# Performance work log

Hardware: AMD Instinct MI355X
Metric: run time of the kernel (lower is better)

## Reference

```python
import jax, jax.numpy as jnp
import numpy as np

B, S, E = 2, 2048, 1024
D_ATTN, H = 1024, 16
HD = D_ATTN // H
SCALE = 1.0 / np.sqrt(D_ATTN)
ROPE_BASE = 10000.0


def setup_inputs() -> dict:
    key = jax.random.key(0)
    ks = jax.random.split(key, 7)
    def w(k, shape, scale):
        return jax.random.normal(k, shape, dtype=jnp.float32) * scale
    return {
        "q": w(ks[0], (B, S, E), 1.0),
        "k": w(ks[1], (B, S, E), 1.0),
        "v": w(ks[2], (B, S, E), 1.0),
        "Wq": w(ks[3], (D_ATTN, E), E ** -0.5),
        "Wk": w(ks[4], (D_ATTN, E), E ** -0.5),
        "Wv": w(ks[5], (D_ATTN, E), E ** -0.5),
        "Wo": w(ks[6], (E, D_ATTN), D_ATTN ** -0.5),
    }


def _rope(x):
    # x: [B, H, S, HD]; interleaved-pair rotary embedding over the seq axis
    s, d = x.shape[2], x.shape[3]
    half = d // 2
    inv_freq = 1.0 / (ROPE_BASE ** (jnp.arange(half, dtype=jnp.float32) * 2.0 / d))
    ang = jnp.arange(s, dtype=jnp.float32)[:, None] * inv_freq[None, :]  # [S, half]
    cos, sin = jnp.cos(ang), jnp.sin(ang)
    xr = x.reshape(x.shape[:-1] + (half, 2))
    x0, x1 = xr[..., 0], xr[..., 1]
    o0 = x0 * cos - x1 * sin
    o1 = x0 * sin + x1 * cos
    return jnp.stack([o0, o1], axis=-1).reshape(x.shape)


def reference(q, k, v, Wq, Wk, Wv, Wo):
    # linear projections (nn.Linear with weight [out, in]): y = x @ W^T
    qh = (q @ Wq.T).reshape(B, S, H, HD).transpose(0, 2, 1, 3)  # [B,H,S,HD]
    kh = (k @ Wk.T).reshape(B, S, H, HD).transpose(0, 2, 1, 3)
    vh = (v @ Wv.T).reshape(B, S, H, HD).transpose(0, 2, 1, 3)
    qh = _rope(qh)
    kh = _rope(kh)
    # shifted-causal mask: disallow j >= i (diagonal masked), except (0,0) allowed
    i = jnp.arange(S)[:, None]
    j = jnp.arange(S)[None, :]
    masked = j >= i                              # triu incl. diagonal
    masked = masked.at[0, 0].set(False)          # keep (0,0) so row 0 isn't all -inf
    scores = jnp.einsum("bhsd,bhtd->bhst", qh, kh) * SCALE
    scores = jnp.where(masked, -jnp.inf, scores)
    probs = jax.nn.softmax(scores, axis=-1)      # dropout omitted (eval mode)
    ctx = jnp.einsum("bhst,bhtd->bhsd", probs, vh)
    ctx = ctx.transpose(0, 2, 1, 3).reshape(B, S, D_ATTN)
    return ctx @ Wo.T
```

## Files before the change

### kernel.cpp

```cpp
#include <hip/hip_runtime.h>
#include <hip/hip_bf16.h>

#define BATCH 2
#define SEQ   2048
#define EMB   1024
#define DATTN 1024
#define NH    16
#define HD    64
#define MM    (BATCH*SEQ)
#define SCALE 0.03125f
#define MINIT -1.0e30f
#define ROPE_COEF 0.41524101186f

using bf16x8 = __attribute__((ext_vector_type(8))) short;
using f32x4  = __attribute__((ext_vector_type(4))) float;

__device__ inline short f2bf(float x) {
    __hip_bfloat16 b = __float2bfloat16(x);
    return *reinterpret_cast<short*>(&b);
}

__device__ inline void gl_lds16(const short* g, short* l) {
    __builtin_amdgcn_global_load_lds(
        (const __attribute__((address_space(1))) unsigned int*)g,
        (__attribute__((address_space(3))) unsigned int*)l, 16, 0, 0);
}

__global__ __launch_bounds__(256)
void cvt_all(const float* __restrict__ q, const float* __restrict__ k,
             const float* __restrict__ v,
             const float* __restrict__ Wq, const float* __restrict__ Wk,
             const float* __restrict__ Wv, const float* __restrict__ Wo,
             short* __restrict__ dst)
{
    const long QKV = (long)MM * EMB;
    const long WSZ = (long)DATTN * EMB;
    const long i = ((long)blockIdx.x * 256 + threadIdx.x) * 4;
    const float* s;
    long off;
    if (i < 3 * QKV) {
        const int seg = (int)(i / QKV);
        off = i - (long)seg * QKV;
        s = (seg == 0) ? q : (seg == 1) ? k : v;
    } else {
        const long j = i - 3 * QKV;
        const int seg = (int)(j / WSZ);
        off = j - (long)seg * WSZ;
        s = (seg == 0) ? Wq : (seg == 1) ? Wk : (seg == 2) ? Wv : Wo;
    }
    float4 x = *(const float4*)(s + off);
    short4 y;
    y.x = f2bf(x.x); y.y = f2bf(x.y); y.z = f2bf(x.z); y.w = f2bf(x.w);
    *(short4*)(dst + i) = y;
}

__device__ inline void stage_tile(const short* g, short* lds, int wave, int lane) {
    #pragma unroll
    for (int qq = 0; qq < 2; ++qq) {
        const int r = wave * 32 + qq * 16 + (lane >> 2);
        gl_lds16(g + (long)r * EMB + (lane & 3) * 8, lds + (wave * 2 + qq) * 512);
    }
}

__global__ __launch_bounds__(256)
void gemm_proj_bf16(const short* __restrict__ qb, const short* __restrict__ kb,
                    const short* __restrict__ vb,
                    const short* __restrict__ wqb, const short* __restrict__ wkb,
                    const short* __restrict__ wvb,
                    short* __restrict__ Qb, short* __restrict__ Kb,
                    short* __restrict__ Vtb)
{
    const short* A; const short* B;
    if (blockIdx.z == 0)      { A = qb; B = wqb; }
    else if (blockIdx.z == 1) { A = kb; B = wkb; }
    else                      { A = vb; B = wvb; }

    __shared__ short sA[128 * 32];
    __shared__ short sB[128 * 32];

    const int tid  = threadIdx.x;
    const int wave = tid >> 6, lane = tid & 63;
    const int quad = lane >> 4, l16 = lane & 15;
    const int wm = (wave >> 1) * 64, wn = (wave & 1) * 64;
    const long m0 = (long)blockIdx.x * 128, n0 = (long)blockIdx.y * 128;

    f32x4 acc[4][4];
    #pragma unroll
    for (int i = 0; i < 4; ++i)
        #pragma unroll
        for (int j = 0; j < 4; ++j) acc[i][j] = (f32x4){0.f, 0.f, 0.f, 0.f};

    for (int kt = 0; kt < EMB; kt += 32) {
        __syncthreads();
        stage_tile(A + m0 * EMB + kt, sA, wave, lane);
        stage_tile(B + n0 * EMB + kt, sB, wave, lane);
        __syncthreads();

        bf16x8 af[4], bfr[4];
        #pragma unroll
        for (int rt = 0; rt < 4; ++rt)
            af[rt] = *(const bf16x8*)&sA[(wm + rt * 16 + l16) * 32 + quad * 8];
        #pragma unroll
        for (int ct = 0; ct < 4; ++ct)
            bfr[ct] = *(const bf16x8*)&sB[(wn + ct * 16 + l16) * 32 + quad * 8];
        #pragma unroll
        for (int rt = 0; rt < 4; ++rt)
            #pragma unroll
            for (int ct = 0; ct < 4; ++ct)
                acc[rt][ct] = __builtin_amdgcn_mfma_f32_16x16x32_bf16(
                    af[rt], bfr[ct], acc[rt][ct], 0, 0, 0);
    }

    if (blockIdx.z < 2) {
        short* C = (blockIdx.z == 0) ? Qb : Kb;
        const float scl = (blockIdx.z == 0) ? SCALE : 1.0f;
        const int odd = l16 & 1;
        #pragma unroll
        for (int ct = 0; ct < 4; ++ct) {
            const long col = n0 + wn + ct * 16 + l16;
            const int hh = (int)(col >> 6), dd = (int)(col & (HD - 1));
            const float invf = exp2f(-ROPE_COEF * (float)(dd >> 1));
            #pragma unroll
            for (int rt = 0; rt < 4; ++rt) {
                #pragma unroll
                for (int reg = 0; reg < 4; ++reg) {
                    const long row = m0 + wm + rt * 16 + quad * 4 + reg;
                    const int bb = (int)(row >> 11), ss = (int)(row & (SEQ - 1));
                    const float val = acc[rt][ct][reg];
                    const float prt = __shfl_xor(val, 1, 64);
                    float sn, cs;
                    __sincosf((float)ss * invf, &sn, &cs);
                    const float o = odd ? (prt * sn + val * cs)
                                        : (val * cs - prt * sn);
                    C[(((long)(bb * NH + hh)) << 17) + ((long)ss << 6) + dd] =
                        f2bf(o * scl);
                }
            }
        }
    } else {
        #pragma unroll
        for (int rt = 0; rt < 4; ++rt) {
            #pragma unroll
            for (int ct = 0; ct < 4; ++ct) {
                const long row0 = m0 + wm + rt * 16 + quad * 4;
                const long col  = n0 + wn + ct * 16 + l16;
                const int bb = (int)(row0 >> 11), ss = (int)(row0 & (SEQ - 1));
                const int hh = (int)(col >> 6),   dd = (int)(col & (HD - 1));
                short4 s4;
                s4.x = f2bf(acc[rt][ct][0]); s4.y = f2bf(acc[rt][ct][1]);
                s4.z = f2bf(acc[rt][ct][2]); s4.w = f2bf(acc[rt][ct][3]);
                *(short4*)&Vtb[(((long)(bb * NH + hh)) << 17) + ((long)dd << 11) + ss] = s4;
            }
        }
    }
}

__global__ __launch_bounds__(256)
void gemm_out_bf16(const short* __restrict__ Ab, const short* __restrict__ Bb,
                   float* __restrict__ C)
{
    __shared__ short sA[128 * 32];
    __shared__ short sB[128 * 32];

    const int tid  = threadIdx.x;
    const int wave = tid >> 6, lane = tid & 63;
    const int quad = lane >> 4, l16 = lane & 15;
    const int wm = (wave >> 1) * 64, wn = (wave & 1) * 64;
    const long m0 = (long)blockIdx.x * 128, n0 = (long)blockIdx.y * 128;

    f32x4 acc[4][4];
    #pragma unroll
    for (int i = 0; i < 4; ++i)
        #pragma unroll
        for (int j = 0; j < 4; ++j) acc[i][j] = (f32x4){0.f, 0.f, 0.f, 0.f};

    for (int kt = 0; kt < DATTN; kt += 32) {
        __syncthreads();
        stage_tile(Ab + m0 * DATTN + kt, sA, wave, lane);
        stage_tile(Bb + n0 * DATTN + kt, sB, wave, lane);
        __syncthreads();

        bf16x8 af[4], bfr[4];
        #pragma unroll
        for (int rt = 0; rt < 4; ++rt)
            af[rt] = *(const bf16x8*)&sA[(wm + rt * 16 + l16) * 32 + quad * 8];
        #pragma unroll
        for (int ct = 0; ct < 4; ++ct)
            bfr[ct] = *(const bf16x8*)&sB[(wn + ct * 16 + l16) * 32 + quad * 8];
        #pragma unroll
        for (int rt = 0; rt < 4; ++rt)
            #pragma unroll
            for (int ct = 0; ct < 4; ++ct)
                acc[rt][ct] = __builtin_amdgcn_mfma_f32_16x16x32_bf16(
                    af[rt], bfr[ct], acc[rt][ct], 0, 0, 0);
    }

    #pragma unroll
    for (int rt = 0; rt < 4; ++rt) {
        #pragma unroll
        for (int ct = 0; ct < 4; ++ct) {
            #pragma unroll
            for (int reg = 0; reg < 4; ++reg) {
                const long row = m0 + wm + rt * 16 + quad * 4 + reg;
                const long col = n0 + wn + ct * 16 + l16;
                C[row * EMB + col] = acc[rt][ct][reg];
            }
        }
    }
}

#define LDP 72

__global__ __launch_bounds__(256, 1)
void flash_attn_mfma(const short* __restrict__ Qb,
                     const short* __restrict__ Kb,
                     const short* __restrict__ Vtb,
                     short* __restrict__ ctx)
{
    const int id = blockIdx.x;
    const int r  = id & 7;
    const int q8 = id >> 3;
    const int ts = q8 & 31;
    const int pi = q8 >> 5;
    const int p  = r + 8 * pi;
    const int b  = p >> 4, h = p & 15;
    const int t  = 31 - ts;
    const int tid = threadIdx.x;
    const int wave = tid >> 6, lane = tid & 63;
    const int quad = lane >> 4, l16 = lane & 15;
    const int r0 = t * 64;

    __shared__ short sk2[2][64 * LDP];
    __shared__ short sv2[2][64 * LDP];
    __shared__ short sp[4][16 * LDP];

    const long base = ((long)(b * NH + h)) << 17;

    const int iq = r0 + wave * 16 + l16;
    bf16x8 qf[2];
    #pragma unroll
    for (int tt = 0; tt < 2; ++tt)
        qf[tt] = *(const bf16x8*)(Qb + base + (long)iq * HD + tt * 32 + quad * 8);

    f32x4 acc_o[4];
    #pragma unroll
    for (int ct = 0; ct < 4; ++ct) acc_o[ct] = (f32x4){0.f, 0.f, 0.f, 0.f};
    float mq = MINIT, lq = 0.f;

    const int njt = (t + 2) >> 1;

    #pragma unroll 1
    for (int jt = 0; jt < njt; ++jt) {
        const int jbase = jt * 128;

        __syncthreads();
        #pragma unroll
        for (int c = 0; c < 4; ++c) {
            int cc   = c * 256 + tid;
            int half = cc >> 9;
            int row  = (cc >> 3) & 63;
            int off  = (cc & 7) * 8;
            int4 tK = *(const int4*)(Kb + base
                + (long)(jbase + half * 64 + row) * HD + off);
            *(int4*)&sk2[half][row * LDP + off] = tK;
            int4 tV = *(const int4*)(Vtb + base
                + ((long)row << 11) + jbase + half * 64 + off);
            *(int4*)&sv2[half][row * LDP + off] = tV;
        }
        __syncthreads();

        #pragma unroll
        for (int half = 0; half < 2; ++half) {
            const int jt2 = 2 * jt + half;
            if (jt2 > t) continue;
            const int jb2 = jbase + half * 64;
            const short* skh = sk2[half];
            const short* svh = sv2[half];

            bf16x8 kf[4][2], vf[4][2];
            #pragma unroll
            for (int ct = 0; ct < 4; ++ct) {
                kf[ct][0] = *(const bf16x8*)&skh[(ct * 16 + l16) * LDP + quad * 8];
                kf[ct][1] = *(const bf16x8*)&skh[(ct * 16 + l16) * LDP + 32 + quad * 8];
                vf[ct][0] = *(const bf16x8*)&svh[(ct * 16 + l16) * LDP + quad * 8];
                vf[ct][1] = *(const bf16x8*)&svh[(ct * 16 + l16) * LDP + 32 + quad * 8];
            }

            f32x4 s[4];
            #pragma unroll
            for (int ct = 0; ct < 4; ++ct) {
                f32x4 z = (f32x4){0.f, 0.f, 0.f, 0.f};
                z = __builtin_amdgcn_mfma_f32_16x16x32_bf16(kf[ct][0], qf[0], z, 0, 0, 0);
                z = __builtin_amdgcn_mfma_f32_16x16x32_bf16(kf[ct][1], qf[1], z, 0, 0, 0);
                s[ct] = z;
            }

            if (jt2 == t) {
                #pragma unroll
                for (int ct = 0; ct < 4; ++ct)
                    #pragma unroll
                    for (int rr = 0; rr < 4; ++rr) {
                        const int j = jb2 + ct * 16 + quad * 4 + rr;
                        const bool ok = (j < iq) || (iq == 0 && j == 0);
                        if (!ok) s[ct][rr] = -INFINITY;
                    }
            }

            float mx = MINIT;
            #pragma unroll
            for (int ct = 0; ct < 4; ++ct)
                #pragma unroll
                for (int rr = 0; rr < 4; ++rr) mx = fmaxf(mx, s[ct][rr]);
            mx = fmaxf(mx, __shfl_xor(mx, 16, 64));
            mx = fmaxf(mx, __shfl_xor(mx, 32, 64));
            const float mn = fmaxf(mq, mx);
            const float alpha = __expf(mq - mn);
            mq = mn;
            float ss = 0.f;
            #pragma unroll
            for (int ct = 0; ct < 4; ++ct)
                #pragma unroll
                for (int rr = 0; rr < 4; ++rr) {
                    const float e = __expf(s[ct][rr] - mn);
                    s[ct][rr] = e;
                    ss += e;
                }
            ss += __shfl_xor(ss, 16, 64);
            ss += __shfl_xor(ss, 32, 64);
            lq = lq * alpha + ss;

            short* pw = sp[wave];
            #pragma unroll
            for (int ct = 0; ct < 4; ++ct) {
                short4 p4;
                p4.x = f2bf(s[ct][0]); p4.y = f2bf(s[ct][1]);
                p4.z = f2bf(s[ct][2]); p4.w = f2bf(s[ct][3]);
                *(short4*)&pw[l16 * LDP + ct * 16 + quad * 4] = p4;
            }

            #pragma unroll
            for (int ct = 0; ct < 4; ++ct)
                #pragma unroll
                for (int rr = 0; rr < 4; ++rr) acc_o[ct][rr] *= alpha;

            bf16x8 pf0 = *(const bf16x8*)&pw[l16 * LDP + quad * 8];
            bf16x8 pf1 = *(const bf16x8*)&pw[l16 * LDP + 32 + quad * 8];
            #pragma unroll
            for (int ct = 0; ct < 4; ++ct) {
                acc_o[ct] = __builtin_amdgcn_mfma_f32_16x16x32_bf16(
                    vf[ct][0], pf0, acc_o[ct], 0, 0, 0);
                acc_o[ct] = __builtin_amdgcn_mfma_f32_16x16x32_bf16(
                    vf[ct][1], pf1, acc_o[ct], 0, 0, 0);
            }
        }
    }

    const float inv = 1.f / lq;
    short* orow = ctx + (long)(b * SEQ + iq) * DATTN + h * HD;
    #pragma unroll
    for (int ct = 0; ct < 4; ++ct) {
        short4 o4;
        o4.x = f2bf(acc_o[ct][0] * inv);
        o4.y = f2bf(acc_o[ct][1] * inv);
        o4.z = f2bf(acc_o[ct][2] * inv);
        o4.w = f2bf(acc_o[ct][3] * inv);
        *(short4*)&orow[ct * 16 + quad * 4] = o4;
    }
}

extern "C" void kernel_launch(void* const* d_in, const int* in_sizes, int n_in,
                              void* d_out, int out_size, void* d_ws, size_t ws_size,
                              hipStream_t stream) {
    const float* q  = (const float*)d_in[0];
    const float* k  = (const float*)d_in[1];
    const float* v  = (const float*)d_in[2];
    const float* Wq = (const float*)d_in[3];
    const float* Wk = (const float*)d_in[4];
    const float* Wv = (const float*)d_in[5];
    const float* Wo = (const float*)d_in[6];
    float* out = (float*)d_out;

    const long QKV = (long)MM * EMB;
    const long WSZ = (long)DATTN * EMB;
    short* basep = (short*)d_ws;
    short* qb  = basep;
    short* kb  = qb + QKV;
    short* vb  = kb + QKV;
    short* wqb = vb + QKV;
    short* wkb = wqb + WSZ;
    short* wvb = wkb + WSZ;
    short* wob = wvb + WSZ;
    short* Qb  = wob + WSZ;
    short* Kb  = Qb + QKV;
    short* Vtb = Kb + QKV;
    short* ctx = Vtb + QKV;

    cvt_all<<<16384, 256, 0, stream>>>(q, k, v, Wq, Wk, Wv, Wo, qb);

    gemm_proj_bf16<<<dim3(MM / 128, DATTN / 128, 3), 256, 0, stream>>>(
        qb, kb, vb, wqb, wkb, wvb, Qb, Kb, Vtb);

    flash_attn_mfma<<<1024, 256, 0, stream>>>(Qb, Kb, Vtb, ctx);

    gemm_out_bf16<<<dim3(MM / 128, EMB / 128), 256, 0, stream>>>(ctx, wob, out);
}
```

Baseline: 237.3 us.

## Pair causal query tiles per block and prefetch K/V tiles into registers

Each attention block now handles two query tiles, a short one (ta) and its mirror long one (31-ta). Both share each staged K/V tile, which balances causal work across blocks and halves K/V loads per query. The next K/V stage is loaded into registers while the current tile is computed, overlapping global loads with MFMA work. The launch bound is raised to 2 blocks per CU. The grid halves to 512 blocks, and the doubled accumulators and Q fragments raise register pressure.

After: 274.4 us. 1.16x slower.

```diff
diff --git a/kernel.cpp b/kernel.cpp
--- a/kernel.cpp
+++ b/kernel.cpp
@@ -211,7 +211,7 @@
 
 #define LDP 72
 
-__global__ __launch_bounds__(256, 1)
+__global__ __launch_bounds__(256, 2)
 void flash_attn_mfma(const short* __restrict__ Qb,
                      const short* __restrict__ Kb,
                      const short* __restrict__ Vtb,
@@ -219,61 +219,152 @@
 {
     const int id = blockIdx.x;
     const int r  = id & 7;
-    const int q8 = id >> 3;
-    const int ts = q8 & 31;
-    const int pi = q8 >> 5;
+    const int q6 = id >> 3;
+    const int ta = q6 & 15;
+    const int pi = q6 >> 4;
     const int p  = r + 8 * pi;
     const int b  = p >> 4, h = p & 15;
-    const int t  = 31 - ts;
+    const int tA = ta;
+    const int tB = 31 - ta;
     const int tid = threadIdx.x;
     const int wave = tid >> 6, lane = tid & 63;
     const int quad = lane >> 4, l16 = lane & 15;
-    const int r0 = t * 64;
 
     __shared__ short sk2[2][64 * LDP];
     __shared__ short sv2[2][64 * LDP];
-    __shared__ short sp[4][16 * LDP];
+    __shared__ short spA[4][16 * LDP];
+    __shared__ short spB[4][16 * LDP];
 
     const long base = ((long)(b * NH + h)) << 17;
 
-    const int iq = r0 + wave * 16 + l16;
-    bf16x8 qf[2];
-    #pragma unroll
-    for (int tt = 0; tt < 2; ++tt)
-        qf[tt] = *(const bf16x8*)(Qb + base + (long)iq * HD + tt * 32 + quad * 8);
-
-    f32x4 acc_o[4];
-    #pragma unroll
-    for (int ct = 0; ct < 4; ++ct) acc_o[ct] = (f32x4){0.f, 0.f, 0.f, 0.f};
-    float mq = MINIT, lq = 0.f;
-
-    const int njt = (t + 2) >> 1;
+    const int iqA = tA * 64 + wave * 16 + l16;
+    const int iqB = tB * 64 + wave * 16 + l16;
+    bf16x8 qfA[2], qfB[2];
+    #pragma unroll
+    for (int tt = 0; tt < 2; ++tt) {
+        qfA[tt] = *(const bf16x8*)(Qb + base + (long)iqA * HD + tt * 32 + quad * 8);
+        qfB[tt] = *(const bf16x8*)(Qb + base + (long)iqB * HD + tt * 32 + quad * 8);
+    }
+
+    f32x4 accA[4], accB[4];
+    #pragma unroll
+    for (int ct = 0; ct < 4; ++ct) {
+        accA[ct] = (f32x4){0.f, 0.f, 0.f, 0.f};
+        accB[ct] = (f32x4){0.f, 0.f, 0.f, 0.f};
+    }
+    float mqA = MINIT, lqA = 0.f, mqB = MINIT, lqB = 0.f;
+
+    const int nr = (tB + 2) >> 1;
+
+    auto attn_tile = [&](const bf16x8 (&kf)[4][2], const bf16x8 (&vf)[4][2],
+                         const bf16x8 (&qf)[2], f32x4 (&acc)[4],
+                         float& mq, float& lq, short* pw,
+                         int jb2, int iq, bool diag) {
+        f32x4 s[4];
+        #pragma unroll
+        for (int ct = 0; ct < 4; ++ct) {
+            f32x4 z = (f32x4){0.f, 0.f, 0.f, 0.f};
+            z = __builtin_amdgcn_mfma_f32_16x16x32_bf16(kf[ct][0], qf[0], z, 0, 0, 0);
+            z = __builtin_amdgcn_mfma_f32_16x16x32_bf16(kf[ct][1], qf[1], z, 0, 0, 0);
+            s[ct] = z;
+        }
+
+        if (diag) {
+            #pragma unroll
+            for (int ct = 0; ct < 4; ++ct)
+                #pragma unroll
+                for (int rr = 0; rr < 4; ++rr) {
+                    const int j = jb2 + ct * 16 + quad * 4 + rr;
+                    const bool ok = (j < iq) || (iq == 0 && j == 0);
+                    if (!ok) s[ct][rr] = -INFINITY;
+                }
+        }
+
+        float mx = MINIT;
+        #pragma unroll
+        for (int ct = 0; ct < 4; ++ct)
+            #pragma unroll
+            for (int rr = 0; rr < 4; ++rr) mx = fmaxf(mx, s[ct][rr]);
+        mx = fmaxf(mx, __shfl_xor(mx, 16, 64));
+        mx = fmaxf(mx, __shfl_xor(mx, 32, 64));
+        const float mn = fmaxf(mq, mx);
+        const float alpha = __expf(mq - mn);
+        mq = mn;
+        float ss = 0.f;
+        #pragma unroll
+        for (int ct = 0; ct < 4; ++ct)
+            #pragma unroll
+            for (int rr = 0; rr < 4; ++rr) {
+                const float e = __expf(s[ct][rr] - mn);
+                s[ct][rr] = e;
+                ss += e;
+            }
+        ss += __shfl_xor(ss, 16, 64);
+        ss += __shfl_xor(ss, 32, 64);
+        lq = lq * alpha + ss;
+
+        #pragma unroll
+        for (int ct = 0; ct < 4; ++ct) {
+            short4 p4;
+            p4.x = f2bf(s[ct][0]); p4.y = f2bf(s[ct][1]);
+            p4.z = f2bf(s[ct][2]); p4.w = f2bf(s[ct][3]);
+            *(short4*)&pw[l16 * LDP + ct * 16 + quad * 4] = p4;
+        }
+
+        #pragma unroll
+        for (int ct = 0; ct < 4; ++ct)
+            #pragma unroll
+            for (int rr = 0; rr < 4; ++rr) acc[ct][rr] *= alpha;
+
+        bf16x8 pf0 = *(const bf16x8*)&pw[l16 * LDP + quad * 8];
+        bf16x8 pf1 = *(const bf16x8*)&pw[l16 * LDP + 32 + quad * 8];
+        #pragma unroll
+        for (int ct = 0; ct < 4; ++ct) {
+            acc[ct] = __builtin_amdgcn_mfma_f32_16x16x32_bf16(
+                vf[ct][0], pf0, acc[ct], 0, 0, 0);
+            acc[ct] = __builtin_amdgcn_mfma_f32_16x16x32_bf16(
+                vf[ct][1], pf1, acc[ct], 0, 0, 0);
+        }
+    };
+
+    int4 rK[4], rV[4];
+    auto load_stage = [&](int jt) {
+        const int jbase = jt * 128;
+        #pragma unroll
+        for (int c = 0; c < 4; ++c) {
+            const int cc   = c * 256 + tid;
+            const int half = cc >> 9;
+            const int row  = (cc >> 3) & 63;
+            const int off  = (cc & 7) * 8;
+            rK[c] = *(const int4*)(Kb + base
+                + (long)(jbase + half * 64 + row) * HD + off);
+            rV[c] = *(const int4*)(Vtb + base
+                + ((long)row << 11) + jbase + half * 64 + off);
+        }
+    };
+
+    load_stage(0);
 
     #pragma unroll 1
-    for (int jt = 0; jt < njt; ++jt) {
-        const int jbase = jt * 128;
-
+    for (int jt = 0; jt < nr; ++jt) {
         __syncthreads();
         #pragma unroll
         for (int c = 0; c < 4; ++c) {
-            int cc   = c * 256 + tid;
-            int half = cc >> 9;
-            int row  = (cc >> 3) & 63;
-            int off  = (cc & 7) * 8;
-            int4 tK = *(const int4*)(Kb + base
-                + (long)(jbase + half * 64 + row) * HD + off);
-            *(int4*)&sk2[half][row * LDP + off] = tK;
-            int4 tV = *(const int4*)(Vtb + base
-                + ((long)row << 11) + jbase + half * 64 + off);
-            *(int4*)&sv2[half][row * LDP + off] = tV;
-        }
-        __syncthreads();
+            const int cc   = c * 256 + tid;
+            const int half = cc >> 9;
+            const int row  = (cc >> 3) & 63;
+            const int off  = (cc & 7) * 8;
+            *(int4*)&sk2[half][row * LDP + off] = rK[c];
+            *(int4*)&sv2[half][row * LDP + off] = rV[c];
+        }
+        __syncthreads();
+        if (jt + 1 < nr) load_stage(jt + 1);
 
         #pragma unroll
         for (int half = 0; half < 2; ++half) {
             const int jt2 = 2 * jt + half;
-            if (jt2 > t) continue;
-            const int jb2 = jbase + half * 64;
+            if (jt2 > tB) continue;
+            const int jb2 = jt * 128 + half * 64;
             const short* skh = sk2[half];
             const short* svh = sv2[half];
 
@@ -286,86 +377,29 @@
                 vf[ct][1] = *(const bf16x8*)&svh[(ct * 16 + l16) * LDP + 32 + quad * 8];
             }
 
-            f32x4 s[4];
-            #pragma unroll
-            for (int ct = 0; ct < 4; ++ct) {
-                f32x4 z = (f32x4){0.f, 0.f, 0.f, 0.f};
-                z = __builtin_amdgcn_mfma_f32_16x16x32_bf16(kf[ct][0], qf[0], z, 0, 0, 0);
-                z = __builtin_amdgcn_mfma_f32_16x16x32_bf16(kf[ct][1], qf[1], z, 0, 0, 0);
-                s[ct] = z;
-            }
-
-            if (jt2 == t) {
-                #pragma unroll
-                for (int ct = 0; ct < 4; ++ct)
-                    #pragma unroll
-                    for (int rr = 0; rr < 4; ++rr) {
-                        const int j = jb2 + ct * 16 + quad * 4 + rr;
-                        const bool ok = (j < iq) || (iq == 0 && j == 0);
-                        if (!ok) s[ct][rr] = -INFINITY;
-                    }
-            }
-
-            float mx = MINIT;
-            #pragma unroll
-            for (int ct = 0; ct < 4; ++ct)
-                #pragma unroll
-                for (int rr = 0; rr < 4; ++rr) mx = fmaxf(mx, s[ct][rr]);
-            mx = fmaxf(mx, __shfl_xor(mx, 16, 64));
-            mx = fmaxf(mx, __shfl_xor(mx, 32, 64));
-            const float mn = fmaxf(mq, mx);
-            const float alpha = __expf(mq - mn);
-            mq = mn;
-            float ss = 0.f;
-            #pragma unroll
-            for (int ct = 0; ct < 4; ++ct)
-                #pragma unroll
-                for (int rr = 0; rr < 4; ++rr) {
-                    const float e = __expf(s[ct][rr] - mn);
-                    s[ct][rr] = e;
-                    ss += e;
-                }
-            ss += __shfl_xor(ss, 16, 64);
-            ss += __shfl_xor(ss, 32, 64);
-            lq = lq * alpha + ss;
-
-            short* pw = sp[wave];
-            #pragma unroll
-            for (int ct = 0; ct < 4; ++ct) {
-                short4 p4;
-                p4.x = f2bf(s[ct][0]); p4.y = f2bf(s[ct][1]);
-                p4.z = f2bf(s[ct][2]); p4.w = f2bf(s[ct][3]);
-                *(short4*)&pw[l16 * LDP + ct * 16 + quad * 4] = p4;
-            }
-
-            #pragma unroll
-            for (int ct = 0; ct < 4; ++ct)
-                #pragma unroll
-                for (int rr = 0; rr < 4; ++rr) acc_o[ct][rr] *= alpha;
-
-            bf16x8 pf0 = *(const bf16x8*)&pw[l16 * LDP + quad * 8];
-            bf16x8 pf1 = *(const bf16x8*)&pw[l16 * LDP + 32 + quad * 8];
-            #pragma unroll
-            for (int ct = 0; ct < 4; ++ct) {
-                acc_o[ct] = __builtin_amdgcn_mfma_f32_16x16x32_bf16(
-                    vf[ct][0], pf0, acc_o[ct], 0, 0, 0);
-                acc_o[ct] = __builtin_amdgcn_mfma_f32_16x16x32_bf16(
-                    vf[ct][1], pf1, acc_o[ct], 0, 0, 0);
-            }
-        }
-    }
-
-    const float inv = 1.f / lq;
-    short* orow = ctx + (long)(b * SEQ + iq) * DATTN + h * HD;
-    #pragma unroll
-    for (int ct = 0; ct < 4; ++ct) {
-        short4 o4;
-        o4.x = f2bf(acc_o[ct][0] * inv);
-        o4.y = f2bf(acc_o[ct][1] * inv);
-        o4.z = f2bf(acc_o[ct][2] * inv);
-        o4.w = f2bf(acc_o[ct][3] * inv);
-        *(short4*)&orow[ct * 16 + quad * 4] = o4;
-    }
+            if (jt2 <= tA)
+                attn_tile(kf, vf, qfA, accA, mqA, lqA, spA[wave],
+                          jb2, iqA, jt2 == tA);
+            attn_tile(kf, vf, qfB, accB, mqB, lqB, spB[wave],
+                      jb2, iqB, jt2 == tB);
+        }
+    }
+
+    auto epi = [&](const f32x4 (&acc)[4], float lq, int iq) {
+        const float inv = 1.f / lq;
+        short* orow = ctx + (long)(b * SEQ + iq) * DATTN + h * HD;
+        #pragma unroll
+        for (int ct = 0; ct < 4; ++ct) {
+            short4 o4;
+            o4.x = f2bf(acc[ct][0] * inv);
+            o4.y = f2bf(acc[ct][1] * inv);
+            o4.z = f2bf(acc[ct][2] * inv);
+            o4.w = f2bf(acc[ct][3] * inv);
+            *(short4*)&orow[ct * 16 + quad * 4] = o4;
+        }
+    };
+    epi(accA, lqA, iqA);
+    epi(accB, lqB, iqB);
 }
 
 extern "C" void kernel_launch(void* const* d_in, const int* in_sizes, int n_in,
@@ -400,7 +434,7 @@
     gemm_proj_bf16<<<dim3(MM / 128, DATTN / 128, 3), 256, 0, stream>>>(
         qb, kb, vb, wqb, wkb, wvb, Qb, Kb, Vtb);
 
-    flash_attn_mfma<<<1024, 256, 0, stream>>>(Qb, Kb, Vtb, ctx);
+    flash_attn_mfma<<<512, 256, 0, stream>>>(Qb, Kb, Vtb, ctx);
 
     gemm_out_bf16<<<dim3(MM / 128, EMB / 128), 256, 0, stream>>>(ctx, wob, out);
 }
```

## Double query rows per flash-attention block to reuse K/V tiles

Applied to the files above, without the earlier changes.

Each block now covers 128 query rows instead of 64, and each wave handles two 16-row query tiles that share the same K and V fragments from LDS. This halves the number of blocks and the total global K/V loads, and reuses each LDS fragment read across two MFMA chains. Block scheduling is remapped to a short/long interleave across two halves of the grid, and launch bounds move to two blocks per CU. The cost is more registers per wave, larger P scratch in LDS, and fewer blocks (512) to fill the device.

New measurement: 230.0 us. -3.1%, faster.

```diff
diff --git a/kernel.cpp b/kernel.cpp
--- a/kernel.cpp
+++ b/kernel.cpp
@@ -211,43 +211,55 @@
 
 #define LDP 72
 
-__global__ __launch_bounds__(256, 1)
+__global__ __launch_bounds__(256, 2)
 void flash_attn_mfma(const short* __restrict__ Qb,
                      const short* __restrict__ Kb,
                      const short* __restrict__ Vtb,
                      short* __restrict__ ctx)
 {
-    const int id = blockIdx.x;
-    const int r  = id & 7;
-    const int q8 = id >> 3;
-    const int ts = q8 & 31;
-    const int pi = q8 >> 5;
-    const int p  = r + 8 * pi;
-    const int b  = p >> 4, h = p & 15;
-    const int t  = 31 - ts;
+    const int id  = blockIdx.x;
+    const int hi  = id >> 8;
+    const int idx = id & 255;
+    const int r   = idx & 7;
+    const int s5  = idx >> 3;
+    const int pi  = s5 & 3;
+    const int ts8 = s5 >> 2;
+    const int p   = r + 8 * pi;
+    const int b   = p >> 4, h = p & 15;
+    const int t   = hi ? ts8 : (15 - ts8);
+
     const int tid = threadIdx.x;
     const int wave = tid >> 6, lane = tid & 63;
     const int quad = lane >> 4, l16 = lane & 15;
-    const int r0 = t * 64;
+    const int r0 = t * 128;
 
     __shared__ short sk2[2][64 * LDP];
     __shared__ short sv2[2][64 * LDP];
-    __shared__ short sp[4][16 * LDP];
+    __shared__ short sp[4][32 * LDP];
 
     const long base = ((long)(b * NH + h)) << 17;
 
-    const int iq = r0 + wave * 16 + l16;
-    bf16x8 qf[2];
-    #pragma unroll
-    for (int tt = 0; tt < 2; ++tt)
-        qf[tt] = *(const bf16x8*)(Qb + base + (long)iq * HD + tt * 32 + quad * 8);
-
-    f32x4 acc_o[4];
-    #pragma unroll
-    for (int ct = 0; ct < 4; ++ct) acc_o[ct] = (f32x4){0.f, 0.f, 0.f, 0.f};
-    float mq = MINIT, lq = 0.f;
-
-    const int njt = (t + 2) >> 1;
+    const int iq0 = r0 + wave * 32 + l16;
+    const int iq1 = iq0 + 16;
+    const int dtile = 2 * t + (wave >> 1);
+
+    bf16x8 qf0[2], qf1[2];
+    #pragma unroll
+    for (int tt = 0; tt < 2; ++tt) {
+        qf0[tt] = *(const bf16x8*)(Qb + base + (long)iq0 * HD + tt * 32 + quad * 8);
+        qf1[tt] = *(const bf16x8*)(Qb + base + (long)iq1 * HD + tt * 32 + quad * 8);
+    }
+
+    f32x4 acc0[4], acc1[4];
+    #pragma unroll
+    for (int ct = 0; ct < 4; ++ct) {
+        acc0[ct] = (f32x4){0.f, 0.f, 0.f, 0.f};
+        acc1[ct] = (f32x4){0.f, 0.f, 0.f, 0.f};
+    }
+    float m0 = MINIT, l0 = 0.f;
+    float m1 = MINIT, l1 = 0.f;
+
+    const int njt = t + 1;
 
     #pragma unroll 1
     for (int jt = 0; jt < njt; ++jt) {
@@ -272,99 +284,153 @@
         #pragma unroll
         for (int half = 0; half < 2; ++half) {
             const int jt2 = 2 * jt + half;
-            if (jt2 > t) continue;
+            if (jt2 > dtile) continue;
             const int jb2 = jbase + half * 64;
             const short* skh = sk2[half];
             const short* svh = sv2[half];
 
-            bf16x8 kf[4][2], vf[4][2];
+            f32x4 s0[4], s1[4];
             #pragma unroll
             for (int ct = 0; ct < 4; ++ct) {
-                kf[ct][0] = *(const bf16x8*)&skh[(ct * 16 + l16) * LDP + quad * 8];
-                kf[ct][1] = *(const bf16x8*)&skh[(ct * 16 + l16) * LDP + 32 + quad * 8];
-                vf[ct][0] = *(const bf16x8*)&svh[(ct * 16 + l16) * LDP + quad * 8];
-                vf[ct][1] = *(const bf16x8*)&svh[(ct * 16 + l16) * LDP + 32 + quad * 8];
-            }
-
-            f32x4 s[4];
-            #pragma unroll
-            for (int ct = 0; ct < 4; ++ct) {
-                f32x4 z = (f32x4){0.f, 0.f, 0.f, 0.f};
-                z = __builtin_amdgcn_mfma_f32_16x16x32_bf16(kf[ct][0], qf[0], z, 0, 0, 0);
-                z = __builtin_amdgcn_mfma_f32_16x16x32_bf16(kf[ct][1], qf[1], z, 0, 0, 0);
-                s[ct] = z;
-            }
-
-            if (jt2 == t) {
+                bf16x8 k0 = *(const bf16x8*)&skh[(ct * 16 + l16) * LDP + quad * 8];
+                bf16x8 k1 = *(const bf16x8*)&skh[(ct * 16 + l16) * LDP + 32 + quad * 8];
+                f32x4 z0 = (f32x4){0.f, 0.f, 0.f, 0.f};
+                z0 = __builtin_amdgcn_mfma_f32_16x16x32_bf16(k0, qf0[0], z0, 0, 0, 0);
+                z0 = __builtin_amdgcn_mfma_f32_16x16x32_bf16(k1, qf0[1], z0, 0, 0, 0);
+                s0[ct] = z0;
+                f32x4 z1 = (f32x4){0.f, 0.f, 0.f, 0.f};
+                z1 = __builtin_amdgcn_mfma_f32_16x16x32_bf16(k0, qf1[0], z1, 0, 0, 0);
+                z1 = __builtin_amdgcn_mfma_f32_16x16x32_bf16(k1, qf1[1], z1, 0, 0, 0);
+                s1[ct] = z1;
+            }
+
+            if (jt2 == dtile) {
                 #pragma unroll
                 for (int ct = 0; ct < 4; ++ct)
                     #pragma unroll
                     for (int rr = 0; rr < 4; ++rr) {
                         const int j = jb2 + ct * 16 + quad * 4 + rr;
-                        const bool ok = (j < iq) || (iq == 0 && j == 0);
-                        if (!ok) s[ct][rr] = -INFINITY;
+                        if (!((j < iq0) || (iq0 == 0 && j == 0)))
+                            s0[ct][rr] = -INFINITY;
+                        if (!(j < iq1))
+                            s1[ct][rr] = -INFINITY;
                     }
             }
 
-            float mx = MINIT;
-            #pragma unroll
-            for (int ct = 0; ct < 4; ++ct)
-                #pragma unroll
-                for (int rr = 0; rr < 4; ++rr) mx = fmaxf(mx, s[ct][rr]);
-            mx = fmaxf(mx, __shfl_xor(mx, 16, 64));
-            mx = fmaxf(mx, __shfl_xor(mx, 32, 64));
-            const float mn = fmaxf(mq, mx);
-            const float alpha = __expf(mq - mn);
-            mq = mn;
-            float ss = 0.f;
+            float mx0 = MINIT;
+            #pragma unroll
+            for (int ct = 0; ct < 4; ++ct)
+                #pragma unroll
+                for (int rr = 0; rr < 4; ++rr) mx0 = fmaxf(mx0, s0[ct][rr]);
+            mx0 = fmaxf(mx0, __shfl_xor(mx0, 16, 64));
+            mx0 = fmaxf(mx0, __shfl_xor(mx0, 32, 64));
+            const float mn0 = fmaxf(m0, mx0);
+            const float a0 = __expf(m0 - mn0);
+            m0 = mn0;
+            float ss0 = 0.f;
             #pragma unroll
             for (int ct = 0; ct < 4; ++ct)
                 #pragma unroll
                 for (int rr = 0; rr < 4; ++rr) {
-                    const float e = __expf(s[ct][rr] - mn);
-                    s[ct][rr] = e;
-                    ss += e;
+                    const float e = __expf(s0[ct][rr] - mn0);
+                    s0[ct][rr] = e;
+                    ss0 += e;
                 }
-            ss += __shfl_xor(ss, 16, 64);
-            ss += __shfl_xor(ss, 32, 64);
-            lq = lq * alpha + ss;
-
-            short* pw = sp[wave];
+            ss0 += __shfl_xor(ss0, 16, 64);
+            ss0 += __shfl_xor(ss0, 32, 64);
+            l0 = l0 * a0 + ss0;
+
+            float mx1 = MINIT;
+            #pragma unroll
+            for (int ct = 0; ct < 4; ++ct)
+                #pragma unroll
+                for (int rr = 0; rr < 4; ++rr) mx1 = fmaxf(mx1, s1[ct][rr]);
+            mx1 = fmaxf(mx1, __shfl_xor(mx1, 16, 64));
+            mx1 = fmaxf(mx1, __shfl_xor(mx1, 32, 64));
+            const float mn1 = fmaxf(m1, mx1);
+            const float a1 = __expf(m1 - mn1);
+            m1 = mn1;
+            float ss1 = 0.f;
+            #pragma unroll
+            for (int ct = 0; ct < 4; ++ct)
+                #pragma unroll
+                for (int rr = 0; rr < 4; ++rr) {
+                    const float e = __expf(s1[ct][rr] - mn1);
+                    s1[ct][rr] = e;
+                    ss1 += e;
+                }
+            ss1 += __shfl_xor(ss1, 16, 64);
+            ss1 += __shfl_xor(ss1, 32, 64);
+            l1 = l1 * a1 + ss1;
+
+            short* pw0 = sp[wave];
+            short* pw1 = sp[wave] + 16 * LDP;
             #pragma unroll
             for (int ct = 0; ct < 4; ++ct) {
                 short4 p4;
-                p4.x = f2bf(s[ct][0]); p4.y = f2bf(s[ct][1]);
-                p4.z = f2bf(s[ct][2]); p4.w = f2bf(s[ct][3]);
-                *(short4*)&pw[l16 * LDP + ct * 16 + quad * 4] = p4;
-            }
-
-            #pragma unroll
-            for (int ct = 0; ct < 4; ++ct)
-                #pragma unroll
-                for (int rr = 0; rr < 4; ++rr) acc_o[ct][rr] *= alpha;
-
-            bf16x8 pf0 = *(const bf16x8*)&pw[l16 * LDP + quad * 8];
-            bf16x8 pf1 = *(const bf16x8*)&pw[l16 * LDP + 32 + quad * 8];
+                p4.x = f2bf(s0[ct][0]); p4.y = f2bf(s0[ct][1]);
+                p4.z = f2bf(s0[ct][2]); p4.w = f2bf(s0[ct][3]);
+                *(short4*)&pw0[l16 * LDP + ct * 16 + quad * 4] = p4;
+                short4 q4;
+                q4.x = f2bf(s1[ct][0]); q4.y = f2bf(s1[ct][1]);
+                q4.z = f2bf(s1[ct][2]); q4.w = f2bf(s1[ct][3]);
+                *(short4*)&pw1[l16 * LDP + ct * 16 + quad * 4] = q4;
+            }
+
+            #pragma unroll
+            for (int ct = 0; ct < 4; ++ct)
+                #pragma unroll
+                for (int rr = 0; rr < 4; ++rr) {
+                    acc0[ct][rr] *= a0;
+                    acc1[ct][rr] *= a1;
+                }
+
+            bf16x8 pf00 = *(const bf16x8*)&pw0[l16 * LDP + quad * 8];
+            bf16x8 pf01 = *(const bf16x8*)&pw0[l16 * LDP + 32 + quad * 8];
+            bf16x8 pf10 = *(const bf16x8*)&pw1[l16 * LDP + quad * 8];
+            bf16x8 pf11 = *(const bf16x8*)&pw1[l16 * LDP + 32 + quad * 8];
+
             #pragma unroll
             for (int ct = 0; ct < 4; ++ct) {
-                acc_o[ct] = __builtin_amdgcn_mfma_f32_16x16x32_bf16(
-                    vf[ct][0], pf0, acc_o[ct], 0, 0, 0);
-                acc_o[ct] = __builtin_amdgcn_mfma_f32_16x16x32_bf16(
-                    vf[ct][1], pf1, acc_o[ct], 0, 0, 0);
-            }
-        }
-    }
-
-    const float inv = 1.f / lq;
-    short* orow = ctx + (long)(b * SEQ + iq) * DATTN + h * HD;
-    #pragma unroll
-    for (int ct = 0; ct < 4; ++ct) {
-        short4 o4;
-        o4.x = f2bf(acc_o[ct][0] * inv);
-        o4.y = f2bf(acc_o[ct][1] * inv);
-        o4.z = f2bf(acc_o[ct][2] * inv);
-        o4.w = f2bf(acc_o[ct][3] * inv);
-        *(short4*)&orow[ct * 16 + quad * 4] = o4;
+                bf16x8 v0 = *(const bf16x8*)&svh[(ct * 16 + l16) * LDP + quad * 8];
+                bf16x8 v1 = *(const bf16x8*)&svh[(ct * 16 + l16) * LDP + 32 + quad * 8];
+                acc0[ct] = __builtin_amdgcn_mfma_f32_16x16x32_bf16(
+                    v0, pf00, acc0[ct], 0, 0, 0);
+                acc0[ct] = __builtin_amdgcn_mfma_f32_16x16x32_bf16(
+                    v1, pf01, acc0[ct], 0, 0, 0);
+                acc1[ct] = __builtin_amdgcn_mfma_f32_16x16x32_bf16(
+                    v0, pf10, acc1[ct], 0, 0, 0);
+                acc1[ct] = __builtin_amdgcn_mfma_f32_16x16x32_bf16(
+                    v1, pf11, acc1[ct], 0, 0, 0);
+            }
+        }
+    }
+
+    {
+        const float inv0 = 1.f / l0;
+        short* orow = ctx + (long)(b * SEQ + iq0) * DATTN + h * HD;
+        #pragma unroll
+        for (int ct = 0; ct < 4; ++ct) {
+            short4 o4;
+            o4.x = f2bf(acc0[ct][0] * inv0);
+            o4.y = f2bf(acc0[ct][1] * inv0);
+            o4.z = f2bf(acc0[ct][2] * inv0);
+            o4.w = f2bf(acc0[ct][3] * inv0);
+            *(short4*)&orow[ct * 16 + quad * 4] = o4;
+        }
+    }
+    {
+        const float inv1 = 1.f / l1;
+        short* orow = ctx + (long)(b * SEQ + iq1) * DATTN + h * HD;
+        #pragma unroll
+        for (int ct = 0; ct < 4; ++ct) {
+            short4 o4;
+            o4.x = f2bf(acc1[ct][0] * inv1);
+            o4.y = f2bf(acc1[ct][1] * inv1);
+            o4.z = f2bf(acc1[ct][2] * inv1);
+            o4.w = f2bf(acc1[ct][3] * inv1);
+            *(short4*)&orow[ct * 16 + quad * 4] = o4;
+        }
     }
 }
 
@@ -400,7 +466,7 @@
     gemm_proj_bf16<<<dim3(MM / 128, DATTN / 128, 3), 256, 0, stream>>>(
         qb, kb, vb, wqb, wkb, wvb, Qb, Kb, Vtb);
 
-    flash_attn_mfma<<<1024, 256, 0, stream>>>(Qb, Kb, Vtb, ctx);
+    flash_attn_mfma<<<512, 256, 0, stream>>>(Qb, Kb, Vtb, ctx);
 
     gemm_out_bf16<<<dim3(MM / 128, EMB / 128), 256, 0, stream>>>(ctx, wob, out);
 }
```
